# Kernel optimization log

Measured on AMD Instinct MI355X. Metric: run time of the kernel, lower is better.

Reference implementation:

```python
import jax, jax.numpy as jnp
import numpy as np
import math

H = 16  # number of heads (init kwarg h)
EPS = 1e-6


def _apply_kernel(x, orf):
    # x: [B, h, L, d_k], orf: [m, d_k]
    m, d_k = orf.shape
    proj = jnp.einsum('bhld,md->bhlm', x, orf) / (d_k ** 0.25)
    norm = jnp.sum(x * x, axis=-1, keepdims=True) / (2.0 * math.sqrt(d_k))
    return (jnp.exp(proj - norm) + EPS) / math.sqrt(m)


def setup_inputs() -> dict:
    key = jax.random.key(0)
    ks = jax.random.split(key, 10)
    B, L, D, m = 4, 4096, 1024, 256
    d_k = D // H
    s = 1.0 / math.sqrt(D)
    return {
        'x': jax.random.normal(ks[0], (B, L, D), jnp.float32),
        'Wq': jax.random.normal(ks[1], (D, D), jnp.float32) * s,
        'bq': jax.random.normal(ks[2], (D,), jnp.float32) * s,
        'Wk': jax.random.normal(ks[3], (D, D), jnp.float32) * s,
        'bk': jax.random.normal(ks[4], (D,), jnp.float32) * s,
        'Wv': jax.random.normal(ks[5], (D, D), jnp.float32) * s,
        'bv': jax.random.normal(ks[6], (D,), jnp.float32) * s,
        'Wo': jax.random.normal(ks[7], (D, D), jnp.float32) * s,
        'bo': jax.random.normal(ks[8], (D,), jnp.float32) * s,
        'orf': jax.random.normal(ks[9], (m, d_k), jnp.float32),
    }


def reference(x, Wq, bq, Wk, bk, Wv, bv, Wo, bo, orf):
    B, L, D = x.shape
    d_k = D // H

    def split(y):  # [B, L, D] -> [B, h, L, d_k]
        return y.reshape(B, L, H, d_k).transpose(0, 2, 1, 3)

    q = split(x @ Wq.T + bq)
    k = split(x @ Wk.T + bk)
    v = split(x @ Wv.T + bv)

    q_phi = _apply_kernel(q, orf)  # [B, h, L, m]
    k_phi = _apply_kernel(k, orf)  # [B, h, L, m]

    # FAVOR+ linear attention: O(L*m*d_k)
    kv = jnp.einsum('bhlm,bhld->bhmd', k_phi, v)      # [B, h, m, d_k]
    ksum = jnp.sum(k_phi, axis=2)                      # [B, h, m]
    num = jnp.einsum('bhlm,bhmd->bhld', q_phi, kv)     # [B, h, L, d_k]
    den = jnp.einsum('bhlm,bhm->bhl', q_phi, ksum)     # [B, h, L]
    out = num / den[..., None]

    out = out.transpose(0, 2, 1, 3).reshape(B, L, D)   # concat heads
    return out @ Wo.T + bo
```

## Files before the change

kernel.cpp:

```cpp
#include <hip/hip_runtime.h>
#include <math.h>

#define HH 16
#define BB 4
#define LL 4096
#define DD 1024
#define DK 64
#define MMF 256
#define EPSF 1e-6f
#define KSCALE (0.35355339059327373f * 1.4426950408889634f)
#define NORMSCALE (0.0625f * 1.4426950408889634f)
#define NSPLIT 8
#define LCH (LL / NSPLIT)

typedef __attribute__((ext_vector_type(8))) short bf16x8;
typedef __attribute__((ext_vector_type(4))) float f32x4;
typedef __attribute__((ext_vector_type(8))) unsigned short u16x8;

__device__ __forceinline__ unsigned short f2bf(float f) {
  union { float f; unsigned u; } v; v.f = f;
  unsigned r = v.u + 0x7FFF + ((v.u >> 16) & 1);
  return (unsigned short)(r >> 16);
}
__device__ __forceinline__ float bf2f(unsigned short h) {
  union { unsigned u; float f; } v; v.u = ((unsigned)h) << 16;
  return v.f;
}
__device__ __forceinline__ f32x4 mfma16(bf16x8 a, bf16x8 b, f32x4 c) {
  return __builtin_amdgcn_mfma_f32_16x16x32_bf16(a, b, c, 0, 0, 0);
}
__device__ __forceinline__ void gload16(const unsigned short* g, unsigned short* l) {
  __builtin_amdgcn_global_load_lds(
      (const __attribute__((address_space(1))) void*)g,
      (__attribute__((address_space(3))) void*)l, 16, 0, 0);
}
#define SWZ(row, col) ((col) ^ (((row) & 7) << 3))

__global__ __launch_bounds__(256) void cvt_bf16(
    const float* __restrict__ src, unsigned short* __restrict__ dst, int n) {
  int i = (blockIdx.x * 256 + threadIdx.x) * 4;
  if (i < n) {
    float4 v = *(const float4*)&src[i];
    ushort4 o;
    o.x = f2bf(v.x); o.y = f2bf(v.y); o.z = f2bf(v.z); o.w = f2bf(v.w);
    *(ushort4*)&dst[i] = o;
  }
}

__global__ __launch_bounds__(256) void cvt_bf16_w(
    const float* __restrict__ W0, const float* __restrict__ W1,
    const float* __restrict__ W2, const float* __restrict__ W3,
    unsigned short* __restrict__ D0, unsigned short* __restrict__ D1,
    unsigned short* __restrict__ D2, unsigned short* __restrict__ D3) {
  const float* s;
  unsigned short* d;
  switch (blockIdx.y) {
    case 0: s = W0; d = D0; break;
    case 1: s = W1; d = D1; break;
    case 2: s = W2; d = D2; break;
    default: s = W3; d = D3; break;
  }
  int i = (blockIdx.x * 256 + threadIdx.x) * 4;
  float4 v = *(const float4*)&s[i];
  ushort4 o;
  o.x = f2bf(v.x); o.y = f2bf(v.y); o.z = f2bf(v.z); o.w = f2bf(v.w);
  *(ushort4*)&d[i] = o;
}

__global__ __launch_bounds__(256) void cvt_orf(
    const float* __restrict__ src, unsigned short* __restrict__ hi,
    unsigned short* __restrict__ lo, int n) {
  int i = blockIdx.x * 256 + threadIdx.x;
  if (i < n) {
    float f = src[i] * KSCALE;
    unsigned short h = f2bf(f);
    hi[i] = h;
    lo[i] = f2bf(f - bf2f(h));
  }
}

template <int MODE>
__global__ __launch_bounds__(256) void gemm_mfma(
    const unsigned short* __restrict__ A, const unsigned short* __restrict__ W,
    const float* __restrict__ bias, float* __restrict__ Cf,
    unsigned short* __restrict__ C1, unsigned short* __restrict__ C2,
    float* __restrict__ Cn, int M, int N, int K) {
  __shared__ __align__(16) char smem[4 * 32 * 68 * 4];
  unsigned short* As = (unsigned short*)smem;
  unsigned short* Bs = (unsigned short*)(smem + 16384);
  const int tid = threadIdx.x, lane = tid & 63;
  const int w = tid >> 6, wr = w >> 1, wc = w & 1;
  const int g = lane >> 4, li = lane & 15;
  const int flat = blockIdx.y * gridDim.x + blockIdx.x;
  const int xcd = flat & 7, loc = flat >> 3;
  const int m0 = ((xcd << 4) + (loc & 15)) * 128;
  const int n0 = (loc >> 4) * 128;

  f32x4 acc[4][4] = {};
  const int srow8 = lane >> 3;
  const int scol  = ((lane & 7) ^ srow8) << 3;
  const unsigned short* Ag = A + (size_t)(m0 + w * 32 + srow8) * K + scol;
  const unsigned short* Wg = W + (size_t)(n0 + w * 32 + srow8) * K + scol;

  for (int k0 = 0; k0 < K; k0 += 64) {
    __syncthreads();
#pragma unroll
    for (int j = 0; j < 4; ++j) {
      gload16(Ag + (size_t)j * 8 * K + k0, &As[(w * 32 + j * 8) * 64]);
      gload16(Wg + (size_t)j * 8 * K + k0, &Bs[(w * 32 + j * 8) * 64]);
    }
    __syncthreads();
    const int sx = (li & 7) << 3;
#pragma unroll
    for (int kk = 0; kk < 2; ++kk) {
      const int c = (kk * 32 + g * 8) ^ sx;
      bf16x8 af[4], bfr[4];
#pragma unroll
      for (int i = 0; i < 4; ++i)
        af[i] = *(const bf16x8*)&As[(wr * 64 + i * 16 + li) * 64 + c];
#pragma unroll
      for (int j = 0; j < 4; ++j)
        bfr[j] = *(const bf16x8*)&Bs[(wc * 64 + j * 16 + li) * 64 + c];
#pragma unroll
      for (int i = 0; i < 4; ++i)
#pragma unroll
        for (int j = 0; j < 4; ++j)
          acc[i][j] = mfma16(af[i], bfr[j], acc[i][j]);
    }
  }

  __syncthreads();
  float* ep = (float*)smem + w * (32 * 68);
  const int head = (n0 + wc * 64) >> 6;
  const int rbase = m0 + wr * 64;
  const int b = rbase >> 12;

  if (MODE == 2) {
#pragma unroll
    for (int jh = 0; jh < 2; ++jh) {
#pragma unroll
      for (int i2 = 0; i2 < 2; ++i2) {
        const int i = jh * 2 + i2;
#pragma unroll
        for (int j = 0; j < 4; ++j) {
          const float bz = bias[n0 + wc * 64 + j * 16 + li];
#pragma unroll
          for (int r = 0; r < 4; ++r)
            ep[(i2 * 16 + 4 * g + r) * 68 + j * 16 + li] = acc[i][j][r] + bz;
        }
      }
      const int rrow = lane >> 3, cc = lane & 7;
#pragma unroll
      for (int p = 0; p < 4; ++p) {
        const int row = p * 8 + rrow;
        float v[8];
        *(f32x4*)&v[0] = *(const f32x4*)&ep[row * 68 + cc * 8];
        *(f32x4*)&v[4] = *(const f32x4*)&ep[row * 68 + cc * 8 + 4];
        float np = 0.f;
        u16x8 hv, lv;
#pragma unroll
        for (int e = 0; e < 8; ++e) {
          float vv = v[e];
          np += vv * vv;
          unsigned short h = f2bf(vv);
          hv[e] = h;
          lv[e] = f2bf(vv - bf2f(h));
        }
        const int lg = (rbase + jh * 32 + row) & 4095;
        const size_t rowb = (size_t)(b * 16 + head) * 4096 + lg;
        *(u16x8*)&C1[rowb * 64 + cc * 8] = hv;
        *(u16x8*)&C2[rowb * 64 + cc * 8] = lv;
        np += __shfl_xor(np, 1);
        np += __shfl_xor(np, 2);
        np += __shfl_xor(np, 4);
        if (cc == 0) Cn[rowb] = np * NORMSCALE;
      }
    }
  } else if (MODE == 1) {
#pragma unroll
    for (int jh = 0; jh < 2; ++jh) {
#pragma unroll
      for (int i = 0; i < 4; ++i)
#pragma unroll
        for (int j2 = 0; j2 < 2; ++j2) {
          const int j = jh * 2 + j2;
          const float bz = bias[n0 + wc * 64 + j * 16 + li];
          f32x4 t;
          t[0] = acc[i][j][0] + bz; t[1] = acc[i][j][1] + bz;
          t[2] = acc[i][j][2] + bz; t[3] = acc[i][j][3] + bz;
          *(f32x4*)&ep[(j2 * 16 + li) * 68 + i * 16 + 4 * g] = t;
        }
      const int rd = lane >> 3, cc = lane & 7;
#pragma unroll
      for (int p = 0; p < 4; ++p) {
        const int dl = p * 8 + rd;
        float v[8];
        *(f32x4*)&v[0] = *(const f32x4*)&ep[dl * 68 + cc * 8];
        *(f32x4*)&v[4] = *(const f32x4*)&ep[dl * 68 + cc * 8 + 4];
        u16x8 hv;
#pragma unroll
        for (int e = 0; e < 8; ++e) hv[e] = f2bf(v[e]);
        const int dh = jh * 32 + dl;
        const int lg = rbase & 4095;
        *(u16x8*)&C1[((size_t)(b * 16 + head) * 64 + dh) * 4096 + lg + cc * 8] = hv;
      }
    }
  } else {
#pragma unroll
    for (int jh = 0; jh < 2; ++jh) {
#pragma unroll
      for (int i2 = 0; i2 < 2; ++i2) {
        const int i = jh * 2 + i2;
#pragma unroll
        for (int j = 0; j < 4; ++j) {
          const float bz = bias[n0 + wc * 64 + j * 16 + li];
#pragma unroll
          for (int r = 0; r < 4; ++r)
            ep[(i2 * 16 + 4 * g + r) * 68 + j * 16 + li] = acc[i][j][r] + bz;
        }
      }
      const int rrow = lane >> 4, cc = lane & 15;
#pragma unroll
      for (int p = 0; p < 8; ++p) {
        const int row = p * 4 + rrow;
        f32x4 v = *(const f32x4*)&ep[row * 68 + cc * 4];
        *(f32x4*)&Cf[(size_t)(rbase + jh * 32 + row) * 1024 + n0 + wc * 64 + cc * 4] = v;
      }
    }
  }
}

__global__ __launch_bounds__(256, 2) void kv_mfma(
    const unsigned short* __restrict__ khi, const unsigned short* __restrict__ klo,
    const float* __restrict__ knorms, const unsigned short* __restrict__ vt,
    const unsigned short* __restrict__ orfhi, const unsigned short* __restrict__ orflo,
    float* __restrict__ pkv, float* __restrict__ pksum) {
  __shared__ __align__(16) unsigned short KsHi[64 * 64], KsLo[64 * 64];
  __shared__ __align__(16) unsigned short VT[64 * 64], KphiT[64 * 64];
  __shared__ float ns[64];
  const int tid = threadIdx.x, lane = tid & 63, w = tid >> 6;
  const int g = lane >> 4, li = lane & 15;
  const int bh = blockIdx.x, sp = blockIdx.y;
  const int srow8 = lane >> 3;
  const int scol  = ((lane & 7) ^ srow8) << 3;
  const int sx = (li & 7) << 3;

  bf16x8 oh[4][2], ol[4][2];
#pragma unroll
  for (int p = 0; p < 4; ++p)
#pragma unroll
    for (int kk = 0; kk < 2; ++kk) {
      const size_t o = (size_t)(p * 64 + w * 16 + li) * 64 + kk * 32 + g * 8;
      oh[p][kk] = *(const bf16x8*)&orfhi[o];
      ol[p][kk] = *(const bf16x8*)&orflo[o];
    }

  f32x4 kvacc[4][4] = {};
  float ksacc[4][4] = {};

  for (int c = 0; c < LCH / 64; ++c) {
    const int l0 = sp * LCH + c * 64;
    __syncthreads();
    {
      const size_t kb = ((size_t)bh * 4096 + l0 + w * 16 + srow8) * 64 + scol;
      gload16(khi + kb, &KsHi[(w * 16) * 64]);
      gload16(khi + kb + 8 * 64, &KsHi[(w * 16 + 8) * 64]);
      gload16(klo + kb, &KsLo[(w * 16) * 64]);
      gload16(klo + kb + 8 * 64, &KsLo[(w * 16 + 8) * 64]);
      const size_t vb = ((size_t)bh * 64 + w * 16 + srow8) * 4096 + l0 + scol;
      gload16(vt + vb, &VT[(w * 16) * 64]);
      gload16(vt + vb + (size_t)8 * 4096, &VT[(w * 16 + 8) * 64]);
      if (tid < 64) ns[tid] = knorms[(size_t)bh * 4096 + l0 + tid];
    }
    __syncthreads();

#pragma unroll
    for (int p = 0; p < 4; ++p) {
      f32x4 pr[4] = {};
      __builtin_amdgcn_s_setprio(1);
#pragma unroll
      for (int kk = 0; kk < 2; ++kk) {
        const int cx = (kk * 32 + g * 8) ^ sx;
#pragma unroll
        for (int lf = 0; lf < 4; ++lf) {
          const bf16x8 bh2 = *(const bf16x8*)&KsHi[(lf * 16 + li) * 64 + cx];
          const bf16x8 bl2 = *(const bf16x8*)&KsLo[(lf * 16 + li) * 64 + cx];
          pr[lf] = mfma16(oh[p][kk], bh2, pr[lf]);
          pr[lf] = mfma16(oh[p][kk], bl2, pr[lf]);
          pr[lf] = mfma16(ol[p][kk], bh2, pr[lf]);
        }
      }
      __builtin_amdgcn_s_setprio(0);
#pragma unroll
      for (int lf = 0; lf < 4; ++lf) {
        const float nrm = ns[lf * 16 + li];
#pragma unroll
        for (int r = 0; r < 4; ++r) {
          float phi = exp2f(pr[lf][r] - nrm) + EPSF;
          ksacc[p][r] += phi;
          const int row = w * 16 + 4 * g + r;
          KphiT[row * 64 + SWZ(row, lf * 16 + li)] = f2bf(phi);
        }
      }
      __builtin_amdgcn_s_setprio(1);
#pragma unroll
      for (int kk = 0; kk < 2; ++kk) {
        const int cx = (kk * 32 + g * 8) ^ sx;
        const bf16x8 a = *(const bf16x8*)&KphiT[(w * 16 + li) * 64 + cx];
#pragma unroll
        for (int df = 0; df < 4; ++df) {
          const bf16x8 bv = *(const bf16x8*)&VT[(df * 16 + li) * 64 + cx];
          kvacc[p][df] = mfma16(a, bv, kvacc[p][df]);
        }
      }
      __builtin_amdgcn_s_setprio(0);
    }
  }
  float* kvo = pkv + ((size_t)sp * 64 + bh) * (MMF * DK);
#pragma unroll
  for (int p = 0; p < 4; ++p)
#pragma unroll
    for (int df = 0; df < 4; ++df)
#pragma unroll
      for (int r = 0; r < 4; ++r)
        kvo[(p * 64 + w * 16 + 4 * g + r) * DK + df * 16 + li] = kvacc[p][df][r];

  float* kso = pksum + ((size_t)sp * 64 + bh) * MMF;
#pragma unroll
  for (int p = 0; p < 4; ++p)
#pragma unroll
    for (int r = 0; r < 4; ++r) {
      float s = ksacc[p][r];
      s += __shfl_xor(s, 1); s += __shfl_xor(s, 2);
      s += __shfl_xor(s, 4); s += __shfl_xor(s, 8);
      if (li == 0) kso[p * 64 + w * 16 + 4 * g + r] = s;
    }
}

__global__ __launch_bounds__(256) void reduce_parts(
    const float* __restrict__ pkv, unsigned short* __restrict__ kvT,
    const float* __restrict__ pks, float* __restrict__ ksg) {
  const int id = blockIdx.x * 256 + threadIdx.x;
  {
    const int bh = id >> 12, rest = id & 4095;
    const int m0 = (rest >> 6) << 2, d = rest & 63;
    float s0 = 0.f, s1 = 0.f, s2 = 0.f, s3 = 0.f;
#pragma unroll
    for (int sp = 0; sp < NSPLIT; ++sp) {
      const float* p = pkv + (size_t)(sp * 64 + bh) * (MMF * DK) + d;
      s0 += p[(m0 + 0) * DK]; s1 += p[(m0 + 1) * DK];
      s2 += p[(m0 + 2) * DK]; s3 += p[(m0 + 3) * DK];
    }
    ushort4 o;
    o.x = f2bf(s0); o.y = f2bf(s1); o.z = f2bf(s2); o.w = f2bf(s3);
    *(ushort4*)&kvT[((size_t)bh * DK + d) * MMF + m0] = o;
  }
  if (id < 4096) {
    float4 s = {0.f, 0.f, 0.f, 0.f};
#pragma unroll
    for (int sp = 0; sp < NSPLIT; ++sp) {
      float4 v = *(const float4*)&pks[(size_t)sp * 64 * MMF + id * 4];
      s.x += v.x; s.y += v.y; s.z += v.z; s.w += v.w;
    }
    *(float4*)&ksg[id * 4] = s;
  }
}

__global__ __launch_bounds__(512, 4) void qattn_mfma(
    const unsigned short* __restrict__ qhi, const unsigned short* __restrict__ qlo,
    const float* __restrict__ qnorms,
    const unsigned short* __restrict__ orfhi,
    const unsigned short* __restrict__ kvT, const float* __restrict__ ksg,
    unsigned short* __restrict__ attn) {
  __shared__ __align__(16) unsigned short OHi[256 * 64];
  __shared__ __align__(16) unsigned short KvTs[64 * 256];
  __shared__ __align__(16) unsigned short Qphi[8][16 * 64];
  const int tid = threadIdx.x, lane = tid & 63, w = tid >> 6;
  const int g = lane >> 4, li = lane & 15;
  const int bh = blockIdx.x, lb = blockIdx.y;
  const int b = bh >> 4, h = bh & 15;
  const int srow8 = lane >> 3;
  const int scol  = ((lane & 7) ^ srow8) << 3;
  const int sx = (li & 7) << 3;

#pragma unroll
  for (int q = 0; q < 4; ++q) {
    const size_t o = (size_t)(w * 32 + q * 8 + srow8) * 64 + scol;
    gload16(orfhi + o, &OHi[(w * 32 + q * 8) * 64]);
  }
  {
    const int srow2 = lane >> 5;
#pragma unroll
    for (int q = 0; q < 4; ++q) {
      const int d0 = w * 8 + q * 2, dr = d0 + srow2;
      gload16(kvT + ((size_t)bh * DK + dr) * MMF + (((lane & 31) ^ (dr & 7)) << 3),
              &KvTs[d0 * 256]);
    }
  }

  float ksr[4][4];
#pragma unroll
  for (int p = 0; p < 4; ++p)
#pragma unroll
    for (int mf = 0; mf < 4; ++mf)
      ksr[p][mf] = ksg[(size_t)bh * MMF + p * 64 + mf * 16 + li];
  const float4 nr =
      *(const float4*)&qnorms[(size_t)bh * 4096 + lb * 128 + w * 16 + 4 * g];
  bf16x8 qh[2], ql[2];
  {
    const size_t qr = ((size_t)bh * 4096 + lb * 128 + w * 16 + li) * 64 + g * 8;
    qh[0] = *(const bf16x8*)&qhi[qr];
    qh[1] = *(const bf16x8*)&qhi[qr + 32];
    ql[0] = *(const bf16x8*)&qlo[qr];
    ql[1] = *(const bf16x8*)&qlo[qr + 32];
  }
  __syncthreads();

  f32x4 numacc[4] = {};
  float denacc[4] = {};

#pragma unroll
  for (int p = 0; p < 4; ++p) {
    f32x4 pr[4] = {};
    __builtin_amdgcn_s_setprio(1);
#pragma unroll
    for (int kk = 0; kk < 2; ++kk) {
      const int cx = (kk * 32 + g * 8) ^ sx;
#pragma unroll
      for (int mf = 0; mf < 4; ++mf) {
        const int row = p * 64 + mf * 16 + li;
        const bf16x8 bh2 = *(const bf16x8*)&OHi[row * 64 + cx];
        pr[mf] = mfma16(qh[kk], bh2, pr[mf]);
        pr[mf] = mfma16(ql[kk], bh2, pr[mf]);
      }
    }
    __builtin_amdgcn_s_setprio(0);
#pragma unroll
    for (int mf = 0; mf < 4; ++mf) {
      const float ks = ksr[p][mf];
#pragma unroll
      for (int r = 0; r < 4; ++r) {
        float phi = exp2f(pr[mf][r] - nr[r]) + EPSF;
        denacc[r] += phi * ks;
        const int row = 4 * g + r;
        Qphi[w][row * 64 + SWZ(row, mf * 16 + li)] = f2bf(phi);
      }
    }
    __builtin_amdgcn_s_setprio(1);
#pragma unroll
    for (int kk = 0; kk < 2; ++kk) {
      const int cx = (kk * 32 + g * 8) ^ sx;
      const bf16x8 a = *(const bf16x8*)&Qphi[w][li * 64 + cx];
#pragma unroll
      for (int df = 0; df < 4; ++df) {
        const bf16x8 bv = *(const bf16x8*)
            &KvTs[(df * 16 + li) * 256 + (((p * 8 + kk * 4 + g) ^ (li & 7)) << 3)];
        numacc[df] = mfma16(a, bv, numacc[df]);
      }
    }
    __builtin_amdgcn_s_setprio(0);
  }
  float den[4];
#pragma unroll
  for (int r = 0; r < 4; ++r) {
    float s = denacc[r];
    s += __shfl_xor(s, 1); s += __shfl_xor(s, 2);
    s += __shfl_xor(s, 4); s += __shfl_xor(s, 8);
    den[r] = s;
  }
  unsigned short* ab =
      attn + ((size_t)b * 4096 + lb * 128) * 1024 + h * 64;
#pragma unroll
  for (int df = 0; df < 4; ++df)
#pragma unroll
    for (int r = 0; r < 4; ++r)
      ab[(size_t)(w * 16 + 4 * g + r) * 1024 + df * 16 + li] =
          f2bf(numacc[df][r] / den[r]);
}

extern "C" void kernel_launch(void* const* d_in, const int* in_sizes, int n_in,
                              void* d_out, int out_size, void* d_ws, size_t ws_size,
                              hipStream_t stream) {
  (void)in_sizes; (void)n_in; (void)out_size; (void)ws_size;
  const float* x   = (const float*)d_in[0];
  const float* Wq  = (const float*)d_in[1];
  const float* bq  = (const float*)d_in[2];
  const float* Wk  = (const float*)d_in[3];
  const float* bk  = (const float*)d_in[4];
  const float* Wv  = (const float*)d_in[5];
  const float* bv  = (const float*)d_in[6];
  const float* Wo  = (const float*)d_in[7];
  const float* bo  = (const float*)d_in[8];
  const float* orf = (const float*)d_in[9];
  float* out = (float*)d_out;

  const size_t ND = (size_t)BB * LL * DD;
  char* base = (char*)d_ws;
  size_t off = 0;
  auto alloc = [&](size_t bytes) -> char* {
    char* p = base + off;
    off += (bytes + 255) & ~(size_t)255;
    return p;
  };
  unsigned short* wqbf   = (unsigned short*)alloc((size_t)DD * DD * 2);
  unsigned short* wkbf   = (unsigned short*)alloc((size_t)DD * DD * 2);
  unsigned short* wvbf   = (unsigned short*)alloc((size_t)DD * DD * 2);
  unsigned short* wobf   = (unsigned short*)alloc((size_t)DD * DD * 2);
  unsigned short* orfhi  = (unsigned short*)alloc((size_t)MMF * DK * 2);
  unsigned short* orflo  = (unsigned short*)alloc((size_t)MMF * DK * 2);
  unsigned short* xbf    = (unsigned short*)alloc(ND * 2);
  unsigned short* qhi    = (unsigned short*)alloc(ND * 2);
  unsigned short* qlo    = (unsigned short*)alloc(ND * 2);
  unsigned short* khi    = (unsigned short*)alloc(ND * 2);
  unsigned short* klo    = (unsigned short*)alloc(ND * 2);
  unsigned short* vtbuf  = (unsigned short*)alloc(ND * 2);
  float*          qnorms = (float*)alloc((size_t)64 * LL * 4);
  float*          knorms = (float*)alloc((size_t)64 * LL * 4);
  float*          pksum  = (float*)alloc((size_t)NSPLIT * 64 * MMF * 4);
  unsigned short* kvT    = (unsigned short*)alloc((size_t)64 * DK * MMF * 2);
  float*          ksg    = (float*)alloc((size_t)64 * MMF * 4);
  float*          pkv    = (float*)xbf;
  unsigned short* attnbf = khi;

  cvt_bf16<<<16384, 256, 0, stream>>>(x, xbf, (int)ND);
  cvt_bf16_w<<<dim3(1024, 4), 256, 0, stream>>>(Wq, Wk, Wv, Wo,
                                                wqbf, wkbf, wvbf, wobf);
  cvt_orf<<<64, 256, 0, stream>>>(orf, orfhi, orflo, MMF * DK);

  dim3 gg(128, 8);
  gemm_mfma<2><<<gg, 256, 0, stream>>>(xbf, wqbf, bq, (float*)0, qhi, qlo,
                                       qnorms, BB * LL, DD, DD);
  gemm_mfma<2><<<gg, 256, 0, stream>>>(xbf, wkbf, bk, (float*)0, khi, klo,
                                       knorms, BB * LL, DD, DD);
  gemm_mfma<1><<<gg, 256, 0, stream>>>(xbf, wvbf, bv, (float*)0, vtbuf,
                                       (unsigned short*)0, (float*)0,
                                       BB * LL, DD, DD);

  kv_mfma<<<dim3(64, NSPLIT), 256, 0, stream>>>(khi, klo, knorms, vtbuf,
                                                orfhi, orflo, pkv, pksum);
  reduce_parts<<<1024, 256, 0, stream>>>(pkv, kvT, pksum, ksg);
  qattn_mfma<<<dim3(64, 32), 512, 0, stream>>>(qhi, qlo, qnorms, orfhi,
                                               kvT, ksg, attnbf);

  gemm_mfma<0><<<gg, 256, 0, stream>>>(attnbf, wobf, bo, out, (unsigned short*)0,
                                       (unsigned short*)0, (float*)0,
                                       BB * LL, DD, DD);
}
```

Measured before the change: 341.9 us.

## Double-buffer LDS tiles in MFMA GEMM to overlap global loads with compute

The GEMM main loop now uses two LDS buffers (64KB total) and prefetches the next K-tile with direct global-to-LDS loads while the current tile feeds the MFMAs. Explicit vmcnt waits and raw s_barrier replace the paired __syncthreads. This aims to hide global memory latency behind matrix compute, at the cost of doubling LDS use, which may lower occupancy to fewer blocks per CU.

```diff
diff --git a/kernel.cpp b/kernel.cpp
--- a/kernel.cpp
+++ b/kernel.cpp
@@ -85,9 +85,8 @@
     const float* __restrict__ bias, float* __restrict__ Cf,
     unsigned short* __restrict__ C1, unsigned short* __restrict__ C2,
     float* __restrict__ Cn, int M, int N, int K) {
-  __shared__ __align__(16) char smem[4 * 32 * 68 * 4];
-  unsigned short* As = (unsigned short*)smem;
-  unsigned short* Bs = (unsigned short*)(smem + 16384);
+  __shared__ __align__(16) char smem[65536];
+  unsigned short* S = (unsigned short*)smem;
   const int tid = threadIdx.x, lane = tid & 63;
   const int w = tid >> 6, wr = w >> 1, wc = w & 1;
   const int g = lane >> 4, li = lane & 15;
@@ -101,15 +100,30 @@
   const int scol  = ((lane & 7) ^ srow8) << 3;
   const unsigned short* Ag = A + (size_t)(m0 + w * 32 + srow8) * K + scol;
   const unsigned short* Wg = W + (size_t)(n0 + w * 32 + srow8) * K + scol;
-
-  for (int k0 = 0; k0 < K; k0 += 64) {
-    __syncthreads();
-#pragma unroll
-    for (int j = 0; j < 4; ++j) {
-      gload16(Ag + (size_t)j * 8 * K + k0, &As[(w * 32 + j * 8) * 64]);
-      gload16(Wg + (size_t)j * 8 * K + k0, &Bs[(w * 32 + j * 8) * 64]);
-    }
-    __syncthreads();
+  const int nt = K >> 6;
+
+#pragma unroll
+  for (int j = 0; j < 4; ++j) {
+    gload16(Ag + (size_t)j * 8 * K, S + (w * 32 + j * 8) * 64);
+    gload16(Wg + (size_t)j * 8 * K, S + 8192 + (w * 32 + j * 8) * 64);
+  }
+
+  for (int t = 0; t < nt; ++t) {
+    const int co = (t & 1) << 14;
+    const int no = co ^ 16384;
+    if (t + 1 < nt) {
+      const int k1 = (t + 1) << 6;
+#pragma unroll
+      for (int j = 0; j < 4; ++j) {
+        gload16(Ag + (size_t)j * 8 * K + k1, S + no + (w * 32 + j * 8) * 64);
+        gload16(Wg + (size_t)j * 8 * K + k1, S + no + 8192 + (w * 32 + j * 8) * 64);
+      }
+      asm volatile("s_waitcnt vmcnt(8)" ::: "memory");
+    } else {
+      asm volatile("s_waitcnt vmcnt(0)" ::: "memory");
+    }
+    __builtin_amdgcn_s_barrier();
+
     const int sx = (li & 7) << 3;
 #pragma unroll
     for (int kk = 0; kk < 2; ++kk) {
@@ -117,19 +131,20 @@
       bf16x8 af[4], bfr[4];
 #pragma unroll
       for (int i = 0; i < 4; ++i)
-        af[i] = *(const bf16x8*)&As[(wr * 64 + i * 16 + li) * 64 + c];
+        af[i] = *(const bf16x8*)&S[co + (wr * 64 + i * 16 + li) * 64 + c];
 #pragma unroll
       for (int j = 0; j < 4; ++j)
-        bfr[j] = *(const bf16x8*)&Bs[(wc * 64 + j * 16 + li) * 64 + c];
+        bfr[j] = *(const bf16x8*)&S[co + 8192 + (wc * 64 + j * 16 + li) * 64 + c];
 #pragma unroll
       for (int i = 0; i < 4; ++i)
 #pragma unroll
         for (int j = 0; j < 4; ++j)
           acc[i][j] = mfma16(af[i], bfr[j], acc[i][j]);
     }
-  }
-
-  __syncthreads();
+    asm volatile("s_waitcnt lgkmcnt(0)" ::: "memory");
+    __builtin_amdgcn_s_barrier();
+  }
+
   float* ep = (float*)smem + w * (32 * 68);
   const int head = (n0 + wc * 64) >> 6;
   const int rbase = m0 + wr * 64;
```

New measurement: 312.9 us. 1.09x faster.
